# Kernel optimization log

Measured on AMD Instinct MI355X. Metric: run time of the kernel, lower is better.

The kernel has to match this reference:

```python
import jax, jax.numpy as jnp
import numpy as np

B, H, Q_TOK, D = 8, 12, 577, 64
N_SIDE = 24  # 24x24 = 576 patches, +1 CLS row/col -> 577


def _pairwise_dists():
    rows, cols = np.indices((N_SIDE, N_SIDE))
    idx = np.stack([rows.flatten(), cols.flatten()], axis=-1).astype(np.float32)  # (576, 2)
    d = idx[:, None, :] - idx[None, :, :]  # (576, 576, 2)
    d = np.pad(d, ((1, 0), (1, 0), (0, 0)))  # zero-pad CLS token row/col -> (577, 577, 2)
    return jnp.asarray(d)


def setup_inputs() -> dict:
    key = jax.random.key(0)
    ks = jax.random.split(key, 4)
    query = jax.random.normal(ks[0], (B, H, Q_TOK, D), jnp.float32)
    W1 = jax.random.normal(ks[1], (D, 64), jnp.float32) * 0.05
    b1 = jnp.zeros((64,), jnp.float32)
    W2 = jax.random.normal(ks[2], (64, 3), jnp.float32) * 0.05
    b2 = jnp.zeros((3,), jnp.float32)
    # uniform noise for RelaxedBernoulli reparameterized sample
    u = jax.random.uniform(ks[3], (B, H, Q_TOK, Q_TOK), jnp.float32, 1e-6, 1.0 - 1e-6)
    temperature = jnp.ones((1,), jnp.float32)
    return {"query": query, "W1": W1, "b1": b1, "W2": W2, "b2": b2,
            "dists": _pairwise_dists(), "u": u, "temperature": temperature}


def reference(query, W1, b1, W2, b2, dists, u, temperature):
    # sigma MLP: Linear -> exact GELU -> Linear, per (b,h,q) token
    hdn = jax.nn.gelu(query @ W1 + b1, approximate=False)
    sig = hdn @ W2 + b2  # (b,h,q,3)
    sy = jnp.exp(sig[..., 0]) + 1.0
    sx = jnp.exp(sig[..., 1]) + 1.0
    rho = jnp.tanh(sig[..., 2]) * 0.99
    cov = sy * sx * rho
    # 2x2 covariance matrix per query: [[sy^2, sy*sx*rho],[sy*sx*rho, sx^2]]
    Sigma = jnp.stack([jnp.stack([sy * sy, cov], -1),
                       jnp.stack([cov, sx * sx], -1)], -2)  # (b,h,q,2,2)
    # closed-form 2x2 inverse (same math as torch.linalg.inv)
    det = (sy * sx) ** 2 * (1.0 - rho * rho)
    inv00 = (sx * sx) / det
    inv11 = (sy * sy) / det
    inv01 = -cov / det
    dy = dists[..., 0]  # (q,k)
    dx = dists[..., 1]
    # Mahalanobis quadratic form, fused (no (b,h,q,k,2,2) intermediates)
    quad = (inv00[..., None] * (dy * dy)
            + 2.0 * inv01[..., None] * (dy * dx)
            + inv11[..., None] * (dx * dx))  # (b,h,q,k)
    kernel = jnp.exp(-0.5 * quad)
    probs = kernel / jnp.max(kernel, axis=-1, keepdims=True)
    probs = jnp.minimum(probs, 1.0)
    # RelaxedBernoulli rsample: sigmoid((logit(p) + logistic_noise) / T)
    logits = jnp.log(probs) - jnp.log1p(-probs)
    noise = jnp.log(u) - jnp.log1p(-u)
    mask = jax.nn.sigmoid((logits + noise) / temperature[0])
    return mask, Sigma
```

## Files before the change

### kernel.cpp

```cpp
#include <hip/hip_runtime.h>
#include <math.h>

constexpr int BB = 8, HH = 12, QT = 577, DD = 64;
constexpr int NTOK = BB * HH * QT;
constexpr long long MASK_ELEMS = (long long)NTOK * QT;
constexpr int NBH = BB * HH;
constexpr int ROWS_PER_WAVE = 8;
constexpr int ROWS_PER_BLOCK = 4 * ROWS_PER_WAVE;
constexpr int CHUNKS = NBH / ROWS_PER_BLOCK;

using f4 = __attribute__((ext_vector_type(4))) float;

__global__ __launch_bounds__(256)
void mlp_sigma(const float* __restrict__ query,
               const float* __restrict__ W1,
               const float* __restrict__ b1,
               const float* __restrict__ W2,
               const float* __restrict__ b2,
               f4* __restrict__ Sig)
{
    const int token = (blockIdx.x * 256 + threadIdx.x) >> 6;
    const int lane  = threadIdx.x & 63;
    if (token >= NTOK) return;

    const float qv = query[(size_t)token * DD + lane];
    float acc = b1[lane];
#pragma unroll
    for (int i = 0; i < DD; ++i)
        acc = fmaf(__shfl(qv, i), W1[i * DD + lane], acc);
    const float h = 0.5f * acc * (1.0f + erff(acc * 0.7071067811865476f));

    float p0 = h * W2[lane * 3 + 0];
    float p1 = h * W2[lane * 3 + 1];
    float p2 = h * W2[lane * 3 + 2];
#pragma unroll
    for (int off = 32; off > 0; off >>= 1) {
        p0 += __shfl_xor(p0, off);
        p1 += __shfl_xor(p1, off);
        p2 += __shfl_xor(p2, off);
    }
    if (lane == 0) {
        const float sy  = expf(p0 + b2[0]) + 1.0f;
        const float sx  = expf(p1 + b2[1]) + 1.0f;
        const float rho = tanhf(p2 + b2[2]) * 0.99f;
        const float cov = sy * sx * rho;
        f4 s; s.x = sy * sy; s.y = cov; s.z = cov; s.w = sx * sx;
        Sig[token] = s;
    }
}

__global__ __launch_bounds__(256)
void mask_rows_v(const float* __restrict__ u,
                 const float* __restrict__ temp,
                 float* __restrict__ out)
{
    __shared__ f4 G4[640];

    const f4* __restrict__ Sig = (const f4*)(out + MASK_ELEMS);
    const int q     = blockIdx.x;
    const int chunk = blockIdx.y;
    const int wave  = threadIdx.x >> 6;
    const int lane  = threadIdx.x & 63;

    {
        const int qm1 = (q > 0) ? q - 1 : 0;
        const int qr  = (int)((unsigned)qm1 / 24u);
        const int qc  = qm1 - qr * 24;
        const float fqr = (float)qr, fqc = (float)qc;
        const bool qz = (q == 0);
        for (int k = threadIdx.x; k < QT; k += 256) {
            const int km1 = (k > 0) ? k - 1 : 0;
            const int kr  = (int)((unsigned)km1 / 24u);
            const int kc  = km1 - kr * 24;
            float dy = fqr - (float)kr;
            float dx = fqc - (float)kc;
            if (qz | (k == 0)) { dy = 0.0f; dx = 0.0f; }
            f4 g; g.x = dy * dy; g.y = dy * dx; g.z = dx * dx; g.w = 0.0f;
            G4[(k & 3) * 160 + (k >> 2)] = g;
        }
    }
    __syncthreads();

    const float invT = 1.0f / temp[0];
    const int bh0 = chunk * ROWS_PER_BLOCK + wave * ROWS_PER_WAVE;

#pragma unroll 1
    for (int r = 0; r < ROWS_PER_WAVE; ++r) {
        const int token = (bh0 + r) * QT + q;
        const f4 S = Sig[token];
        const float rdet = __fdividef(1.0f, fmaf(S.x, S.w, -S.y * S.y));
        const float j0 =  0.5f * S.w * rdet;
        const float j1 = -S.y * rdet;
        const float j2 =  0.5f * S.x * rdet;

        const unsigned base = (unsigned)token * (unsigned)QT;
        const int h  = (int)((0u - base) & 3u);
        const int NV = (QT - h) >> 2;

        const float* __restrict__ up = u   + base + h;
        float*       __restrict__ mp = out + base + h;

        int bc[4];
#pragma unroll
        for (int c = 0; c < 4; ++c)
            bc[c] = ((h + c) & 3) * 160 + ((h + c) >> 2);

#pragma unroll
        for (int p = 0; p < 3; ++p) {
            const int idx = p * 64 + lane;
            if (idx < NV) {
                const f4 uu = *(const f4*)(up + 4 * idx);
                f4 m4;
#pragma unroll
                for (int c = 0; c < 4; ++c) {
                    const f4 g = G4[bc[c] + idx];
                    const float hq = fmaxf(
                        fmaf(j2, g.z, fmaf(j1, g.y, j0 * g.x)), 0.0f);
                    const float E  = __expf(hq);
                    const float a  = E - 1.0f;
                    const float uv = uu[c];
                    float m = __fdividef(uv, fmaf(a, 1.0f - uv, uv));
                    if (invT != 1.0f) {
                        const float rr = __fdividef(a * (1.0f - uv), uv);
                        m = __fdividef(1.0f, 1.0f + __expf(__logf(rr) * invT));
                    }
                    m4[c] = m;
                }
                __builtin_nontemporal_store(m4, (f4*)(mp + 4 * idx));
            }
        }

        const int scnt = QT - 4 * NV;
        if (lane < scnt) {
            const int k = (lane < h) ? lane : (h + 4 * NV + (lane - h));
            const f4 g = G4[(k & 3) * 160 + (k >> 2)];
            const float hq = fmaxf(
                fmaf(j2, g.z, fmaf(j1, g.y, j0 * g.x)), 0.0f);
            const float E  = __expf(hq);
            const float a  = E - 1.0f;
            const float uv = u[base + k];
            float m = __fdividef(uv, fmaf(a, 1.0f - uv, uv));
            if (invT != 1.0f) {
                const float rr = __fdividef(a * (1.0f - uv), uv);
                m = __fdividef(1.0f, 1.0f + __expf(__logf(rr) * invT));
            }
            __builtin_nontemporal_store(m, out + base + k);
        }
    }
}

extern "C" void kernel_launch(void* const* d_in, const int* in_sizes, int n_in,
                              void* d_out, int out_size, void* d_ws, size_t ws_size,
                              hipStream_t stream) {
    const float* query = (const float*)d_in[0];
    const float* W1    = (const float*)d_in[1];
    const float* b1    = (const float*)d_in[2];
    const float* W2    = (const float*)d_in[3];
    const float* b2    = (const float*)d_in[4];
    const float* u     = (const float*)d_in[6];
    const float* temp  = (const float*)d_in[7];
    float* out = (float*)d_out;

    f4* Sig = (f4*)(out + MASK_ELEMS);
    mlp_sigma<<<dim3(NTOK / 4), dim3(256), 0, stream>>>(query, W1, b1, W2, b2, Sig);
    mask_rows_v<<<dim3(QT, CHUNKS), dim3(256), 0, stream>>>(u, temp, out);
}
```

Before: 313.2 us.

## Assign one row per wave with 512-thread blocks and template the temperature path

Restructures the mask kernel so each wave handles a single (b,h) row, with 8 waves per 512-thread block, replacing the earlier loop of 8 rows per wave in 256-thread blocks. The Sigma load and address setup are hoisted ahead of the shared-memory table build so they overlap with it. The temperature branch is made wave-uniform through readfirstlane and turned into a template choice, keeping the T=1 inner loop free of the general-path code. The grid grows to more blocks, each of which rebuilds the distance table, in exchange for more memory-level parallelism and less serial per-wave work.

```diff
diff --git a/kernel.cpp b/kernel.cpp
--- a/kernel.cpp
+++ b/kernel.cpp
@@ -5,9 +5,8 @@
 constexpr int NTOK = BB * HH * QT;
 constexpr long long MASK_ELEMS = (long long)NTOK * QT;
 constexpr int NBH = BB * HH;
-constexpr int ROWS_PER_WAVE = 8;
-constexpr int ROWS_PER_BLOCK = 4 * ROWS_PER_WAVE;
-constexpr int CHUNKS = NBH / ROWS_PER_BLOCK;
+constexpr int WAVES_PER_BLOCK = 8;
+constexpr int CHUNKS = NBH / WAVES_PER_BLOCK;
 
 using f4 = __attribute__((ext_vector_type(4))) float;
 
@@ -49,10 +48,58 @@
     }
 }
 
-__global__ __launch_bounds__(256)
-void mask_rows_v(const float* __restrict__ u,
-                 const float* __restrict__ temp,
-                 float* __restrict__ out)
+template<bool T1>
+__device__ __forceinline__ float mask_elem(float g0, float g1, float g2,
+                                           float j0, float j1, float j2,
+                                           float uv, float invT)
+{
+    const float hq = fmaxf(fmaf(j2, g2, fmaf(j1, g1, j0 * g0)), 0.0f);
+    const float E  = __expf(hq);
+    const float a  = E - 1.0f;
+    if (T1)
+        return __fdividef(uv, fmaf(a, 1.0f - uv, uv));
+    const float rr = __fdividef(a * (1.0f - uv), uv);
+    return __fdividef(1.0f, 1.0f + __expf(__logf(rr) * invT));
+}
+
+template<bool T1>
+__device__ __forceinline__ void do_row(const f4* __restrict__ G4,
+                                       const float* __restrict__ up,
+                                       float* __restrict__ mp,
+                                       const float* __restrict__ u,
+                                       float* __restrict__ out,
+                                       unsigned base, int h, int NV,
+                                       const int* bc, int lane,
+                                       float j0, float j1, float j2, float invT)
+{
+#pragma unroll
+    for (int p = 0; p < 3; ++p) {
+        const int idx = p * 64 + lane;
+        if (idx < NV) {
+            const f4 uu = *(const f4*)(up + 4 * idx);
+            f4 m4;
+#pragma unroll
+            for (int c = 0; c < 4; ++c) {
+                const f4 g = G4[bc[c] + idx];
+                m4[c] = mask_elem<T1>(g.x, g.y, g.z, j0, j1, j2, uu[c], invT);
+            }
+            __builtin_nontemporal_store(m4, (f4*)(mp + 4 * idx));
+        }
+    }
+    const int scnt = QT - 4 * NV;
+    if (lane < scnt) {
+        const int k = (lane < h) ? lane : (h + 4 * NV + (lane - h));
+        const f4 g = G4[(k & 3) * 160 + (k >> 2)];
+        const float m = mask_elem<T1>(g.x, g.y, g.z, j0, j1, j2,
+                                      u[base + k], invT);
+        __builtin_nontemporal_store(m, out + base + k);
+    }
+}
+
+__global__ __launch_bounds__(512)
+void mask_hyb(const float* __restrict__ u,
+              const float* __restrict__ temp,
+              float* __restrict__ out)
 {
     __shared__ f4 G4[640];
 
@@ -62,13 +109,27 @@
     const int wave  = threadIdx.x >> 6;
     const int lane  = threadIdx.x & 63;
 
+    const int token = (chunk * WAVES_PER_BLOCK + wave) * QT + q;
+    const f4 S = Sig[token];
+    const float tval = temp[0];
+
+    const unsigned base = (unsigned)token * (unsigned)QT;
+    const int h  = (int)((0u - base) & 3u);
+    const int NV = (QT - h) >> 2;
+    const float* __restrict__ up = u   + base + h;
+    float*       __restrict__ mp = out + base + h;
+    int bc[4];
+#pragma unroll
+    for (int c = 0; c < 4; ++c)
+        bc[c] = ((h + c) & 3) * 160 + ((h + c) >> 2);
+
     {
         const int qm1 = (q > 0) ? q - 1 : 0;
         const int qr  = (int)((unsigned)qm1 / 24u);
         const int qc  = qm1 - qr * 24;
         const float fqr = (float)qr, fqc = (float)qc;
         const bool qz = (q == 0);
-        for (int k = threadIdx.x; k < QT; k += 256) {
+        for (int k = threadIdx.x; k < QT; k += 512) {
             const int km1 = (k > 0) ? k - 1 : 0;
             const int kr  = (int)((unsigned)km1 / 24u);
             const int kc  = km1 - kr * 24;
@@ -81,72 +142,17 @@
     }
     __syncthreads();
 
-    const float invT = 1.0f / temp[0];
-    const int bh0 = chunk * ROWS_PER_BLOCK + wave * ROWS_PER_WAVE;
+    const float rdet = __fdividef(1.0f, fmaf(S.x, S.w, -S.y * S.y));
+    const float j0 =  0.5f * S.w * rdet;
+    const float j1 = -S.y * rdet;
+    const float j2 =  0.5f * S.x * rdet;
 
-#pragma unroll 1
-    for (int r = 0; r < ROWS_PER_WAVE; ++r) {
-        const int token = (bh0 + r) * QT + q;
-        const f4 S = Sig[token];
-        const float rdet = __fdividef(1.0f, fmaf(S.x, S.w, -S.y * S.y));
-        const float j0 =  0.5f * S.w * rdet;
-        const float j1 = -S.y * rdet;
-        const float j2 =  0.5f * S.x * rdet;
-
-        const unsigned base = (unsigned)token * (unsigned)QT;
-        const int h  = (int)((0u - base) & 3u);
-        const int NV = (QT - h) >> 2;
-
-        const float* __restrict__ up = u   + base + h;
-        float*       __restrict__ mp = out + base + h;
-
-        int bc[4];
-#pragma unroll
-        for (int c = 0; c < 4; ++c)
-            bc[c] = ((h + c) & 3) * 160 + ((h + c) >> 2);
-
-#pragma unroll
-        for (int p = 0; p < 3; ++p) {
-            const int idx = p * 64 + lane;
-            if (idx < NV) {
-                const f4 uu = *(const f4*)(up + 4 * idx);
-                f4 m4;
-#pragma unroll
-                for (int c = 0; c < 4; ++c) {
-                    const f4 g = G4[bc[c] + idx];
-                    const float hq = fmaxf(
-                        fmaf(j2, g.z, fmaf(j1, g.y, j0 * g.x)), 0.0f);
-                    const float E  = __expf(hq);
-                    const float a  = E - 1.0f;
-                    const float uv = uu[c];
-                    float m = __fdividef(uv, fmaf(a, 1.0f - uv, uv));
-                    if (invT != 1.0f) {
-                        const float rr = __fdividef(a * (1.0f - uv), uv);
-                        m = __fdividef(1.0f, 1.0f + __expf(__logf(rr) * invT));
-                    }
-                    m4[c] = m;
-                }
-                __builtin_nontemporal_store(m4, (f4*)(mp + 4 * idx));
-            }
-        }
-
-        const int scnt = QT - 4 * NV;
-        if (lane < scnt) {
-            const int k = (lane < h) ? lane : (h + 4 * NV + (lane - h));
-            const f4 g = G4[(k & 3) * 160 + (k >> 2)];
-            const float hq = fmaxf(
-                fmaf(j2, g.z, fmaf(j1, g.y, j0 * g.x)), 0.0f);
-            const float E  = __expf(hq);
-            const float a  = E - 1.0f;
-            const float uv = u[base + k];
-            float m = __fdividef(uv, fmaf(a, 1.0f - uv, uv));
-            if (invT != 1.0f) {
-                const float rr = __fdividef(a * (1.0f - uv), uv);
-                m = __fdividef(1.0f, 1.0f + __expf(__logf(rr) * invT));
-            }
-            __builtin_nontemporal_store(m, out + base + k);
-        }
-    }
+    const float invT = __int_as_float(__builtin_amdgcn_readfirstlane(
+                           __float_as_int(__fdividef(1.0f, tval))));
+    if (invT == 1.0f)
+        do_row<true >(G4, up, mp, u, out, base, h, NV, bc, lane, j0, j1, j2, invT);
+    else
+        do_row<false>(G4, up, mp, u, out, base, h, NV, bc, lane, j0, j1, j2, invT);
 }
 
 extern "C" void kernel_launch(void* const* d_in, const int* in_sizes, int n_in,
@@ -163,5 +169,5 @@
 
     f4* Sig = (f4*)(out + MASK_ELEMS);
     mlp_sigma<<<dim3(NTOK / 4), dim3(256), 0, stream>>>(query, W1, b1, W2, b2, Sig);
-    mask_rows_v<<<dim3(QT, CHUNKS), dim3(256), 0, stream>>>(u, temp, out);
+    mask_hyb<<<dim3(QT, CHUNKS), dim3(512), 0, stream>>>(u, temp, out);
 }
```

New measurement: 303.2 us. -3.2%, faster.
